# Kernel tuning notes

Hardware: AMD Instinct MI355X
Metric: run time of the kernel (lower is better)

The kernel has to match this reference:

```python
import jax, jax.numpy as jnp
import numpy as np

D_MODEL = 1024
NUM_HEADS = 16
SEQ_LEN = 2048
BATCH = 2
THETA = 10000.0


def apply_rope(x, positions, theta):
    # x: [..., seq, d_k]; positions: [seq]
    dk = x.shape[-1]
    half = dk // 2
    k = jnp.arange(half, dtype=jnp.float32)
    inv_freq = theta ** (-2.0 * k / dk)                 # [half]
    ang = positions.astype(jnp.float32)[:, None] * inv_freq  # [seq, half]
    cos, sin = jnp.cos(ang), jnp.sin(ang)
    xe = x[..., 0::2]   # even members of adjacent pairs
    xo = x[..., 1::2]
    out_e = cos * xe - sin * xo
    out_o = sin * xe + cos * xo
    # interleave pairs back: [..., seq, half, 2] -> [..., seq, dk]
    return jnp.stack([out_e, out_o], axis=-1).reshape(x.shape)


def setup_inputs() -> dict:
    key = jax.random.key(0)
    kx, kq, kk, kv, ko = jax.random.split(key, 5)
    sig = 1.0 / np.sqrt(D_MODEL)
    def tn(k):
        return jnp.clip(jax.random.normal(k, (D_MODEL, D_MODEL), jnp.float32), -3.0, 3.0) * sig
    return {
        "x": jax.random.normal(kx, (BATCH, SEQ_LEN, D_MODEL), jnp.float32),
        "q_proj_weight": tn(kq),
        "k_proj_weight": tn(kk),
        "v_proj_weight": tn(kv),
        "o_proj_weight": tn(ko),
        "token_positions": jnp.arange(SEQ_LEN, dtype=jnp.int32),
    }


def reference(x, q_proj_weight, k_proj_weight, v_proj_weight, o_proj_weight, token_positions):
    h = NUM_HEADS
    d = x.shape[-1]
    dh = d // h
    seq = x.shape[-2]
    Wq = q_proj_weight.reshape(h, dh, d)
    Wk = k_proj_weight.reshape(h, dh, d)
    Wv = v_proj_weight.reshape(h, dh, d)
    Q = jnp.einsum('bsd,hed->bhse', x, Wq)
    K = jnp.einsum('bsd,hed->bhse', x, Wk)
    V = jnp.einsum('bsd,hed->bhse', x, Wv)
    Q = apply_rope(Q, token_positions, THETA)
    K = apply_rope(K, token_positions, THETA)
    scores = jnp.einsum('bhqe,bhke->bhqk', Q, K) / jnp.sqrt(jnp.float32(dh))
    mask = jnp.tril(jnp.ones((seq, seq), dtype=bool))
    scores = jnp.where(mask, scores, -jnp.inf)
    probs = jax.nn.softmax(scores, axis=-1)
    att = jnp.einsum('bhqk,bhke->bhqe', probs, V)       # [b, h, s, dh]
    att = att.transpose(0, 2, 1, 3).reshape(x.shape[0], seq, d)  # concat heads
    return jnp.einsum('bsh,dh->bsd', att, o_proj_weight)
```

## Files before the change

### kernel.cpp

```cpp
#include <hip/hip_runtime.h>
#include <hip/hip_bf16.h>
#include <cstdint>
#include <cstddef>

#define DEV static __device__ __forceinline__

typedef __bf16 bf16x8 __attribute__((ext_vector_type(8)));
typedef float f32x4 __attribute__((ext_vector_type(4)));
typedef unsigned short u16;

static constexpr int BATCH = 2, SEQ = 2048, DM = 1024, NH = 16, DH = 64;
static constexpr int Kdim = 1024;
static constexpr int BS = BATCH * SEQ;

DEV u16 f2b(float f) {
  uint32_t u = __builtin_bit_cast(uint32_t, f);
  u += 0x7FFFu + ((u >> 16) & 1u);
  return (u16)(u >> 16);
}

DEV void gload_lds16(const void* g, void* l) {
  __builtin_amdgcn_global_load_lds((const __attribute__((address_space(1))) void*)g,
                                   (__attribute__((address_space(3))) void*)l, 16, 0, 0);
}

DEV void plswap32(uint32_t& a, uint32_t& b) {
  asm("v_permlane32_swap_b32 %0, %1" : "+v"(a), "+v"(b));
}
DEV void plswap16(uint32_t& a, uint32_t& b) {
  asm("v_permlane16_swap_b32 %0, %1" : "+v"(a), "+v"(b));
}

__global__ __launch_bounds__(256) void cast_all(const float* __restrict__ x,
    const float* __restrict__ wq, const float* __restrict__ wk,
    const float* __restrict__ wv, const float* __restrict__ wo,
    const int* __restrict__ pos,
    u16* __restrict__ xb, u16* __restrict__ wqb, u16* __restrict__ wkb,
    u16* __restrict__ wvb, u16* __restrict__ wob, float2* __restrict__ tab) {
  const int NX = (BATCH * SEQ * DM) / 4;
  const int NW = (DM * DM) / 4;
  const int NT = SEQ * 32;
  int i = blockIdx.x * blockDim.x + threadIdx.x;
  const int stride = gridDim.x * blockDim.x;
  for (; i < NX + 4 * NW + NT; i += stride) {
    if (i < NX + 4 * NW) {
      const float* src; u16* dst; int off;
      if (i < NX) { src = x; dst = xb; off = i; }
      else {
        const int j = i - NX, seg = j >> 18;
        off = j & (NW - 1);
        src = seg == 0 ? wq : seg == 1 ? wk : seg == 2 ? wv : wo;
        dst = seg == 0 ? wqb : seg == 1 ? wkb : seg == 2 ? wvb : wob;
      }
      float4 v = ((const float4*)src)[off];
      ushort4 o;
      o.x = f2b(v.x); o.y = f2b(v.y); o.z = f2b(v.z); o.w = f2b(v.w);
      ((ushort4*)dst)[off] = o;
    } else {
      const int t = i - NX - 4 * NW;
      const int s = t >> 5, j = t & 31;
      const float ang = (float)pos[s] * exp2f((float)j * -0.4152410118609203f);
      float sn, cs;
      sincosf(ang, &sn, &cs);
      tab[t] = make_float2(cs, sn);
    }
  }
}

template <bool OUTF32>
DEV void gemm_core64(const u16* __restrict__ A, const u16* __restrict__ Bm,
                     void* __restrict__ Cout, int ldC, int m0, int n0,
                     u16* __restrict__ As, u16* __restrict__ Bs) {
  const int tid = threadIdx.x;
  const int lane = tid & 63, wid = tid >> 6;
  const int wr = (wid >> 1) * 64, wc = (wid & 1) * 32;
  const int frow = lane & 15, fgrp = lane >> 4;
  constexpr int NK = Kdim / 32;
  f32x4 acc[4][2] = {};

  const int c0 = tid, c1 = tid + 256;
  const int ra0 = c0 >> 2, sa0 = (c0 & 3) ^ ((ra0 >> 1) & 3);
  const int ra1 = c1 >> 2, sa1 = (c1 & 3) ^ ((ra1 >> 1) & 3);
  const size_t gA0 = (size_t)(m0 + ra0) * Kdim + sa0 * 8;
  const size_t gA1 = (size_t)(m0 + ra1) * Kdim + sa1 * 8;
  const size_t gB0 = (size_t)(n0 + ra0) * Kdim + sa0 * 8;

#define GSTAGE(bufi, kofs)                                                      \
  do {                                                                          \
    gload_lds16(A + gA0 + (kofs), As + (bufi) * 4096 + wid * 512);              \
    gload_lds16(A + gA1 + (kofs), As + (bufi) * 4096 + wid * 512 + 2048);       \
    gload_lds16(Bm + gB0 + (kofs), Bs + (bufi) * 2048 + wid * 512);             \
  } while (0)

  GSTAGE(0, 0);
  for (int kt = 0; kt < NK; ++kt) {
    const int buf = kt & 1;
    if (kt + 1 < NK) {
      GSTAGE((kt + 1) & 1, (kt + 1) * 32);
      asm volatile("s_waitcnt vmcnt(3)" ::: "memory");
    } else {
      asm volatile("s_waitcnt vmcnt(0)" ::: "memory");
    }
    __builtin_amdgcn_s_barrier();

    bf16x8 af[4], bfr[2];
#pragma unroll
    for (int i = 0; i < 4; ++i) {
      const int ra = wr + i * 16 + frow;
      af[i] = *(const bf16x8*)((const char*)(As + buf * 4096) + ra * 64 +
                               ((fgrp ^ ((ra >> 1) & 3)) * 16));
    }
#pragma unroll
    for (int f = 0; f < 2; ++f) {
      const int rb = wc + f * 16 + frow;
      bfr[f] = *(const bf16x8*)((const char*)(Bs + buf * 2048) + rb * 64 +
                                ((fgrp ^ ((rb >> 1) & 3)) * 16));
    }
#pragma unroll
    for (int mi = 0; mi < 4; ++mi)
#pragma unroll
      for (int f = 0; f < 2; ++f)
        acc[mi][f] = __builtin_amdgcn_mfma_f32_16x16x32_bf16(af[mi], bfr[f], acc[mi][f], 0, 0, 0);

    __builtin_amdgcn_s_barrier();
  }
#undef GSTAGE

  const int colb = n0 + wc + frow;
  const int rowb = m0 + wr + fgrp * 4;
#pragma unroll
  for (int mi = 0; mi < 4; ++mi)
#pragma unroll
    for (int f = 0; f < 2; ++f)
#pragma unroll
      for (int r = 0; r < 4; ++r) {
        const int row = rowb + mi * 16 + r;
        const int col = colb + f * 16;
        const float v = acc[mi][f][r];
        if (OUTF32) ((float*)Cout)[(size_t)row * ldC + col] = v;
        else        ((u16*)Cout)[(size_t)row * ldC + col] = f2b(v);
      }
}

DEV void qk_core(const u16* __restrict__ xb, const u16* __restrict__ wq,
                 const u16* __restrict__ wk, u16* __restrict__ Qb, u16* __restrict__ Kb,
                 const float2* __restrict__ tab, int m0, int n0,
                 u16* __restrict__ As, u16* __restrict__ Bq, u16* __restrict__ Bk) {
  const int tid = threadIdx.x;
  const int lane = tid & 63, wid = tid >> 6;
  const int wr = (wid >> 1) * 64, wc = (wid & 1) * 32;
  const int frow = lane & 15, fgrp = lane >> 4;
  constexpr int NK = Kdim / 32;
  f32x4 accQ[4][2] = {}, accK[4][2] = {};

  const int c0 = tid, c1 = tid + 256;
  const int ra0 = c0 >> 2, sa0 = (c0 & 3) ^ ((ra0 >> 1) & 3);
  const int ra1 = c1 >> 2, sa1 = (c1 & 3) ^ ((ra1 >> 1) & 3);
  const size_t gA0 = (size_t)(m0 + ra0) * Kdim + sa0 * 8;
  const size_t gA1 = (size_t)(m0 + ra1) * Kdim + sa1 * 8;
  const size_t gB0 = (size_t)(n0 + ra0) * Kdim + sa0 * 8;

#define QKSTAGE(bufi, kofs)                                                     \
  do {                                                                          \
    gload_lds16(xb + gA0 + (kofs), As + (bufi) * 4096 + wid * 512);             \
    gload_lds16(xb + gA1 + (kofs), As + (bufi) * 4096 + wid * 512 + 2048);      \
    gload_lds16(wq + gB0 + (kofs), Bq + (bufi) * 2048 + wid * 512);             \
    gload_lds16(wk + gB0 + (kofs), Bk + (bufi) * 2048 + wid * 512);             \
  } while (0)

  QKSTAGE(0, 0);
  for (int kt = 0; kt < NK; ++kt) {
    const int buf = kt & 1;
    if (kt + 1 < NK) {
      QKSTAGE((kt + 1) & 1, (kt + 1) * 32);
      asm volatile("s_waitcnt vmcnt(4)" ::: "memory");
    } else {
      asm volatile("s_waitcnt vmcnt(0)" ::: "memory");
    }
    __builtin_amdgcn_s_barrier();

    bf16x8 af[4], bq[2], bk[2];
#pragma unroll
    for (int i = 0; i < 4; ++i) {
      const int ra = wr + i * 16 + frow;
      af[i] = *(const bf16x8*)((const char*)(As + buf * 4096) + ra * 64 +
                               ((fgrp ^ ((ra >> 1) & 3)) * 16));
    }
#pragma unroll
    for (int f2 = 0; f2 < 2; ++f2) {
      const int rb = wc + f2 * 16 + frow;
      const int off = rb * 64 + ((fgrp ^ ((rb >> 1) & 3)) * 16);
      bq[f2] = *(const bf16x8*)((const char*)(Bq + buf * 2048) + off);
      bk[f2] = *(const bf16x8*)((const char*)(Bk + buf * 2048) + off);
    }
#pragma unroll
    for (int mi = 0; mi < 4; ++mi)
#pragma unroll
      for (int f2 = 0; f2 < 2; ++f2) {
        accQ[mi][f2] = __builtin_amdgcn_mfma_f32_16x16x32_bf16(af[mi], bq[f2], accQ[mi][f2], 0, 0, 0);
        accK[mi][f2] = __builtin_amdgcn_mfma_f32_16x16x32_bf16(af[mi], bk[f2], accK[mi][f2], 0, 0, 0);
      }

    __builtin_amdgcn_s_barrier();
  }
#undef QKSTAGE

  const int colb = n0 + wc + frow;
  const int rowb = m0 + wr + fgrp * 4;
#pragma unroll
  for (int mi = 0; mi < 4; ++mi)
#pragma unroll
    for (int f2 = 0; f2 < 2; ++f2) {
      const int col = colb + f2 * 16;
      const int jj = (col & 63) >> 1;
      const int odd = col & 1;
#pragma unroll
      for (int r = 0; r < 4; ++r) {
        const int row = rowb + mi * 16 + r;
        const float2 cs_ = tab[(row & (SEQ - 1)) * 32 + jj];
        const float qv = accQ[mi][f2][r];
        const float qp = __shfl_xor(qv, 1);
        const float kv = accK[mi][f2][r];
        const float kp = __shfl_xor(kv, 1);
        float oq = odd ? fmaf(cs_.y, qp, cs_.x * qv) : fmaf(cs_.x, qv, -cs_.y * qp);
        float ok = odd ? fmaf(cs_.y, kp, cs_.x * kv) : fmaf(cs_.x, kv, -cs_.y * kp);
        oq *= 0.18033688011112043f;
        Qb[(size_t)row * DM + col] = f2b(oq);
        Kb[(size_t)row * DM + col] = f2b(ok);
      }
    }
}

__global__ __launch_bounds__(256) void gemm_proj(const u16* __restrict__ xb,
    const u16* __restrict__ wq, const u16* __restrict__ wk, const u16* __restrict__ wv,
    u16* __restrict__ Qb, u16* __restrict__ Kb, u16* __restrict__ Vtb,
    const float2* __restrict__ tab) {
  __shared__ u16 As[2][4096], B1[2][2048], B2[2][2048];
  const int g = blockIdx.x;
  if (g < 512) {
    const int xcd = g & 7, j = g >> 3;
    const int m0 = (xcd * 4 + (j >> 4)) * 128, n0 = (j & 15) * 64;
    qk_core(xb, wq, wk, Qb, Kb, tab, m0, n0, &As[0][0], &B1[0][0], &B2[0][0]);
  } else {
    const int f = g - 512;
    const int xcd = f & 7, j = f >> 3;
    const int m0 = xcd * 128, n0 = j * 64;
    gemm_core64<false>(wv, xb, Vtb, BS, m0, n0, &As[0][0], &B1[0][0]);
  }
}

__global__ __launch_bounds__(256) void gemm_o(const u16* __restrict__ attb,
                                              const u16* __restrict__ wob,
                                              float* __restrict__ out) {
  __shared__ u16 As[2][4096], Bs[2][2048];
  const int f = blockIdx.x;
  const int xcd = f & 7, k = f >> 3;
  const int grp = xcd * 8 + (k >> 3);
  const int m0 = (grp >> 1) * 128;
  const int n0 = ((grp & 1) * 8 + (k & 7)) * 64;
  gemm_core64<true>(attb, wob, out, DM, m0, n0, &As[0][0], &Bs[0][0]);
}

__global__ __launch_bounds__(256, 2) void attn_kernel(const u16* __restrict__ Qb,
                                                      const u16* __restrict__ Kb,
                                                      const u16* __restrict__ Vtb,
                                                      u16* __restrict__ attb) {
  __shared__ __align__(16) unsigned char SM[73728];
  u16* Qs = (u16*)(SM + 65536);
  float* Of = (float*)SM;
  float* Ld = (float*)(SM + 65536);

  const int tid = threadIdx.x, lane = tid & 63, wid = tid >> 6;
  const int flat = (int)blockIdx.x + 16 * (int)blockIdx.y;
  const int orig = (flat & 7) * 64 + (flat >> 3);
  const int xq = orig & 15;
  const int bh = orig >> 4;
  const int b = bh >> 4, h = bh & 15;
  const size_t base_bh = ((size_t)b * SEQ) * DM + h * DH;
  const int frow = lane & 15, fgrp = lane >> 4;
  const int w32 = wid * 32;
  const int swz = (frow & 7) << 4;

  const u16* Ksrcs[4];
  const u16* Vsrcs[4];
#pragma unroll
  for (int i = 0; i < 4; ++i) {
    const int c = tid + i * 256;
    const int rk = c >> 3, s8 = (c & 7) ^ (rk & 7);
    Ksrcs[i] = Kb + base_bh + (size_t)rk * DM + s8 * 8;
    const int rv = c >> 4, s16 = (c & 15) ^ (rv & 7);
    Vsrcs[i] = Vtb + (size_t)(h * DH + rv) * BS + (size_t)b * SEQ + s16 * 8;
  }
  const int cq0 = tid, cq1 = tid + 256;
  const int rq0 = cq0 >> 3, sq0 = (cq0 & 7) ^ (rq0 & 7);
  const int rq1 = cq1 >> 3, sq1 = (cq1 & 7) ^ (rq1 & 7);

#pragma unroll 1
  for (int phase = 0; phase < 2; ++phase) {
    const int qt = phase ? xq : 31 - xq;
    const int q0 = qt * 64;
    const int nkv = (qt >> 1) + 1;

    gload_lds16(Qb + base_bh + (size_t)(q0 + rq0) * DM + sq0 * 8, (char*)SM + 65536 + tid * 16);
    gload_lds16(Qb + base_bh + (size_t)(q0 + rq1) * DM + sq1 * 8, (char*)SM + 69632 + tid * 16);
#pragma unroll
    for (int i = 0; i < 4; ++i) {
      gload_lds16(Ksrcs[i], (char*)SM + wid * 1024 + i * 4096);
      gload_lds16(Vsrcs[i], (char*)SM + 32768 + wid * 1024 + i * 4096);
    }
    __syncthreads();

    bf16x8 qf[4][2];
#pragma unroll
    for (int qs = 0; qs < 4; ++qs)
#pragma unroll
      for (int ks = 0; ks < 2; ++ks) {
        const int byte = ((qs * 16 + frow) * 128 + ks * 64 + fgrp * 16) ^ swz;
        qf[qs][ks] = *(const bf16x8*)((const char*)Qs + byte);
      }

    f32x4 accO[4][4] = {};
    float l_lane[4] = {0.f, 0.f, 0.f, 0.f};

    const u16* Kp[4];
    const u16* Vp[4];
#pragma unroll
    for (int i = 0; i < 4; ++i) { Kp[i] = Ksrcs[i] + (size_t)128 * DM; Vp[i] = Vsrcs[i] + 128; }

    for (int kt = 0; kt < nkv; ++kt) {
      const char* Kc = (const char*)SM + (kt & 1) * 16384;
      const char* Vc = (const char*)SM + 32768 + (kt & 1) * 16384;
      if (kt + 1 < nkv) {
        const int nb = (kt + 1) & 1;
#pragma unroll
        for (int i = 0; i < 4; ++i) {
          gload_lds16(Kp[i], (char*)SM + nb * 16384 + wid * 1024 + i * 4096);
          gload_lds16(Vp[i], (char*)SM + 32768 + nb * 16384 + wid * 1024 + i * 4096);
          Kp[i] += (size_t)128 * DM;
          Vp[i] += 128;
        }
      }

      f32x4 sc[4][2] = {};
      __builtin_amdgcn_s_setprio(1);
#pragma unroll
      for (int tc = 0; tc < 2; ++tc)
#pragma unroll
        for (int ks = 0; ks < 2; ++ks) {
          const int byte = ((w32 + tc * 16 + frow) * 128 + ks * 64 + fgrp * 16) ^ swz;
          const bf16x8 kf = *(const bf16x8*)(Kc + byte);
#pragma unroll
          for (int qs = 0; qs < 4; ++qs)
            sc[qs][tc] = __builtin_amdgcn_mfma_f32_16x16x32_bf16(kf, qf[qs][ks], sc[qs][tc], 0, 0, 0);
        }
      __builtin_amdgcn_s_setprio(0);

      if (kt == nkv - 1) {
        const int kv0 = kt * 128;
#pragma unroll
        for (int qs = 0; qs < 4; ++qs)
#pragma unroll
          for (int tc = 0; tc < 2; ++tc)
#pragma unroll
            for (int r = 0; r < 4; ++r)
              if (kv0 + w32 + tc * 16 + fgrp * 4 + r > q0 + qs * 16 + frow)
                sc[qs][tc][r] = -1e30f;
      }

      bf16x8 pf[4];
#pragma unroll
      for (int qs = 0; qs < 4; ++qs) {
        const float p00 = exp2f(sc[qs][0][0]), p01 = exp2f(sc[qs][0][1]);
        const float p02 = exp2f(sc[qs][0][2]), p03 = exp2f(sc[qs][0][3]);
        const float p10 = exp2f(sc[qs][1][0]), p11 = exp2f(sc[qs][1][1]);
        const float p12 = exp2f(sc[qs][1][2]), p13 = exp2f(sc[qs][1][3]);
        l_lane[qs] += ((p00 + p01) + (p02 + p03)) + ((p10 + p11) + (p12 + p13));
        union { __bf16 bb[2]; uint32_t uu; } c00, c01, c10, c11;
        c00.bb[0] = (__bf16)p00; c00.bb[1] = (__bf16)p01;
        c01.bb[0] = (__bf16)p02; c01.bb[1] = (__bf16)p03;
        c10.bb[0] = (__bf16)p10; c10.bb[1] = (__bf16)p11;
        c11.bb[0] = (__bf16)p12; c11.bb[1] = (__bf16)p13;
        uint32_t a0 = c00.uu, a1 = c01.uu, b0 = c10.uu, b1 = c11.uu;
        plswap32(a0, b0); plswap16(a0, b0);
        plswap32(a1, b1); plswap16(a1, b1);
        union { uint32_t w[4]; bf16x8 v; } pk;
        pk.w[0] = a0; pk.w[1] = a1; pk.w[2] = b0; pk.w[3] = b1;
        pf[qs] = pk.v;
      }

      __builtin_amdgcn_s_setprio(1);
#pragma unroll
      for (int te = 0; te < 4; ++te) {
        const int byte = ((te * 16 + frow) * 256 + wid * 64 + fgrp * 16) ^ swz;
        const bf16x8 vf = *(const bf16x8*)(Vc + byte);
#pragma unroll
        for (int qs = 0; qs < 4; ++qs)
          accO[qs][te] = __builtin_amdgcn_mfma_f32_16x16x32_bf16(pf[qs], vf, accO[qs][te], 0, 0, 0);
      }
      __builtin_amdgcn_s_setprio(0);
      __syncthreads();
    }

    float* myOf = Of + wid * 4096;
#pragma unroll
    for (int qs = 0; qs < 4; ++qs)
#pragma unroll
      for (int te = 0; te < 4; ++te)
#pragma unroll
        for (int r = 0; r < 4; ++r)
          myOf[(qs * 16 + fgrp * 4 + r) * 64 + te * 16 + frow] = accO[qs][te][r];
#pragma unroll
    for (int qs = 0; qs < 4; ++qs) {
      l_lane[qs] += __shfl_xor(l_lane[qs], 16);
      l_lane[qs] += __shfl_xor(l_lane[qs], 32);
    }
    if (fgrp == 0) {
#pragma unroll
      for (int qs = 0; qs < 4; ++qs) Ld[wid * 64 + qs * 16 + frow] = l_lane[qs];
    }
    __syncthreads();

    {
      const int qlb = wid * 16 + fgrp * 4;
#pragma unroll
      for (int i = 0; i < 4; ++i) {
        const int ql = qlb + i;
        f32x4 s = {};
#pragma unroll
        for (int wv = 0; wv < 4; ++wv) {
          const f32x4 t = *(const f32x4*)(Of + wv * 4096 + ql * 64 + frow * 4);
          s += t;
        }
        const float lq = ((Ld[ql] + Ld[64 + ql]) + (Ld[128 + ql] + Ld[192 + ql]));
        const float inv = 1.0f / lq;
        ushort4 o;
        o.x = f2b(s[0] * inv); o.y = f2b(s[1] * inv);
        o.z = f2b(s[2] * inv); o.w = f2b(s[3] * inv);
        *(ushort4*)(attb + base_bh + (size_t)(q0 + ql) * DM + frow * 4) = o;
      }
    }
    __syncthreads();
  }
}

extern "C" void kernel_launch(void* const* d_in, const int* in_sizes, int n_in,
                              void* d_out, int out_size, void* d_ws, size_t ws_size,
                              hipStream_t stream) {
  const float* x  = (const float*)d_in[0];
  const float* wq = (const float*)d_in[1];
  const float* wk = (const float*)d_in[2];
  const float* wv = (const float*)d_in[3];
  const float* wo = (const float*)d_in[4];
  const int* pos  = (const int*)d_in[5];
  float* out = (float*)d_out;
  (void)in_sizes; (void)n_in; (void)out_size; (void)ws_size;

  char* ws = (char*)d_ws;
  const size_t MB = 1024 * 1024;
  u16* xb   = (u16*)(ws);
  u16* wqb  = (u16*)(ws + 8 * MB);
  u16* wkb  = (u16*)(ws + 10 * MB);
  u16* wvb  = (u16*)(ws + 12 * MB);
  u16* wob  = (u16*)(ws + 14 * MB);
  u16* Qb   = (u16*)(ws + 16 * MB);
  u16* Kb   = (u16*)(ws + 24 * MB);
  u16* Vtb  = (u16*)(ws + 32 * MB);
  u16* attb = (u16*)(ws + 40 * MB);
  float2* tab = (float2*)(ws + 40 * MB);

  cast_all<<<2048, 256, 0, stream>>>(x, wq, wk, wv, wo, pos, xb, wqb, wkb, wvb, wob, tab);
  gemm_proj<<<1024, 256, 0, stream>>>(xb, wqb, wkb, wvb, Qb, Kb, Vtb, tab);
  attn_kernel<<<dim3(16, 32), 256, 0, stream>>>(Qb, Kb, Vtb, attb);
  gemm_o<<<512, 256, 0, stream>>>(attb, wob, out);
}
```

Baseline: 112.4 us.

## Single-buffer K/V tiles and halve LDS to raise attention occupancy

Shrinks the attention kernel's shared memory from 72KB to 40KB by dropping K/V double buffering, aliasing Q into the reduction area, and splitting the cross-wave output reduction into two halves. Launch bounds go from 2 to 4 blocks per CU, so more waves are resident to hide latency. In exchange, the next K/V tile is loaded only after compute with an extra barrier, so global loads no longer overlap the MFMA work within a block. Register pressure also tightens under the higher launch bound.

```diff
diff --git a/kernel.cpp b/kernel.cpp
--- a/kernel.cpp
+++ b/kernel.cpp
@@ -261,14 +261,13 @@
   gemm_core64<true>(attb, wob, out, DM, m0, n0, &As[0][0], &Bs[0][0]);
 }
 
-__global__ __launch_bounds__(256, 2) void attn_kernel(const u16* __restrict__ Qb,
+__global__ __launch_bounds__(256, 4) void attn_kernel(const u16* __restrict__ Qb,
                                                       const u16* __restrict__ Kb,
                                                       const u16* __restrict__ Vtb,
                                                       u16* __restrict__ attb) {
-  __shared__ __align__(16) unsigned char SM[73728];
-  u16* Qs = (u16*)(SM + 65536);
+  __shared__ __align__(16) unsigned char SM[40960];
   float* Of = (float*)SM;
-  float* Ld = (float*)(SM + 65536);
+  float* Ld = (float*)(SM + 32768);
 
   const int tid = threadIdx.x, lane = tid & 63, wid = tid >> 6;
   const int flat = (int)blockIdx.x + 16 * (int)blockIdx.y;
@@ -301,12 +300,12 @@
     const int q0 = qt * 64;
     const int nkv = (qt >> 1) + 1;
 
-    gload_lds16(Qb + base_bh + (size_t)(q0 + rq0) * DM + sq0 * 8, (char*)SM + 65536 + tid * 16);
-    gload_lds16(Qb + base_bh + (size_t)(q0 + rq1) * DM + sq1 * 8, (char*)SM + 69632 + tid * 16);
+    gload_lds16(Qb + base_bh + (size_t)(q0 + rq0) * DM + sq0 * 8, (char*)SM + 32768 + wid * 1024);
+    gload_lds16(Qb + base_bh + (size_t)(q0 + rq1) * DM + sq1 * 8, (char*)SM + 32768 + wid * 1024 + 4096);
 #pragma unroll
     for (int i = 0; i < 4; ++i) {
       gload_lds16(Ksrcs[i], (char*)SM + wid * 1024 + i * 4096);
-      gload_lds16(Vsrcs[i], (char*)SM + 32768 + wid * 1024 + i * 4096);
+      gload_lds16(Vsrcs[i], (char*)SM + 16384 + wid * 1024 + i * 4096);
     }
     __syncthreads();
 
@@ -316,31 +315,16 @@
 #pragma unroll
       for (int ks = 0; ks < 2; ++ks) {
         const int byte = ((qs * 16 + frow) * 128 + ks * 64 + fgrp * 16) ^ swz;
-        qf[qs][ks] = *(const bf16x8*)((const char*)Qs + byte);
+        qf[qs][ks] = *(const bf16x8*)((const char*)SM + 32768 + byte);
       }
 
     f32x4 accO[4][4] = {};
     float l_lane[4] = {0.f, 0.f, 0.f, 0.f};
 
-    const u16* Kp[4];
-    const u16* Vp[4];
-#pragma unroll
-    for (int i = 0; i < 4; ++i) { Kp[i] = Ksrcs[i] + (size_t)128 * DM; Vp[i] = Vsrcs[i] + 128; }
+    const char* Kc = (const char*)SM;
+    const char* Vc = (const char*)SM + 16384;
 
     for (int kt = 0; kt < nkv; ++kt) {
-      const char* Kc = (const char*)SM + (kt & 1) * 16384;
-      const char* Vc = (const char*)SM + 32768 + (kt & 1) * 16384;
-      if (kt + 1 < nkv) {
-        const int nb = (kt + 1) & 1;
-#pragma unroll
-        for (int i = 0; i < 4; ++i) {
-          gload_lds16(Kp[i], (char*)SM + nb * 16384 + wid * 1024 + i * 4096);
-          gload_lds16(Vp[i], (char*)SM + 32768 + nb * 16384 + wid * 1024 + i * 4096);
-          Kp[i] += (size_t)128 * DM;
-          Vp[i] += 128;
-        }
-      }
-
       f32x4 sc[4][2] = {};
       __builtin_amdgcn_s_setprio(1);
 #pragma unroll
@@ -399,47 +383,60 @@
       }
       __builtin_amdgcn_s_setprio(0);
       __syncthreads();
-    }
-
-    float* myOf = Of + wid * 4096;
-#pragma unroll
-    for (int qs = 0; qs < 4; ++qs)
-#pragma unroll
-      for (int te = 0; te < 4; ++te)
-#pragma unroll
-        for (int r = 0; r < 4; ++r)
-          myOf[(qs * 16 + fgrp * 4 + r) * 64 + te * 16 + frow] = accO[qs][te][r];
+
+      if (kt + 1 < nkv) {
+        const size_t kvn = (size_t)(kt + 1) * 128;
+#pragma unroll
+        for (int i = 0; i < 4; ++i) {
+          gload_lds16(Ksrcs[i] + kvn * DM, (char*)SM + wid * 1024 + i * 4096);
+          gload_lds16(Vsrcs[i] + kvn, (char*)SM + 16384 + wid * 1024 + i * 4096);
+        }
+        __syncthreads();
+      }
+    }
+
 #pragma unroll
     for (int qs = 0; qs < 4; ++qs) {
       l_lane[qs] += __shfl_xor(l_lane[qs], 16);
       l_lane[qs] += __shfl_xor(l_lane[qs], 32);
     }
-    if (fgrp == 0) {
-#pragma unroll
-      for (int qs = 0; qs < 4; ++qs) Ld[wid * 64 + qs * 16 + frow] = l_lane[qs];
-    }
-    __syncthreads();
-
-    {
-      const int qlb = wid * 16 + fgrp * 4;
-#pragma unroll
-      for (int i = 0; i < 4; ++i) {
-        const int ql = qlb + i;
+#pragma unroll 1
+    for (int hh = 0; hh < 2; ++hh) {
+      float* myOf = Of + wid * 2048;
+#pragma unroll
+      for (int q2 = 0; q2 < 2; ++q2) {
+        const int qs = hh * 2 + q2;
+#pragma unroll
+        for (int te = 0; te < 4; ++te)
+#pragma unroll
+          for (int r = 0; r < 4; ++r)
+            myOf[(q2 * 16 + fgrp * 4 + r) * 64 + te * 16 + frow] = accO[qs][te][r];
+      }
+      if (fgrp == 0) {
+#pragma unroll
+        for (int q2 = 0; q2 < 2; ++q2)
+          Ld[wid * 32 + q2 * 16 + frow] = l_lane[hh * 2 + q2];
+      }
+      __syncthreads();
+
+#pragma unroll
+      for (int ii = 0; ii < 2; ++ii) {
+        const int qll = wid * 8 + fgrp * 2 + ii;
         f32x4 s = {};
+        float lq = 0.f;
 #pragma unroll
         for (int wv = 0; wv < 4; ++wv) {
-          const f32x4 t = *(const f32x4*)(Of + wv * 4096 + ql * 64 + frow * 4);
-          s += t;
+          s += *(const f32x4*)(Of + wv * 2048 + qll * 64 + frow * 4);
+          lq += Ld[wv * 32 + qll];
         }
-        const float lq = ((Ld[ql] + Ld[64 + ql]) + (Ld[128 + ql] + Ld[192 + ql]));
         const float inv = 1.0f / lq;
         ushort4 o;
         o.x = f2b(s[0] * inv); o.y = f2b(s[1] * inv);
         o.z = f2b(s[2] * inv); o.w = f2b(s[3] * inv);
-        *(ushort4*)(attb + base_bh + (size_t)(q0 + ql) * DM + frow * 4) = o;
-      }
-    }
-    __syncthreads();
+        *(ushort4*)(attb + base_bh + (size_t)(q0 + hh * 32 + qll) * DM + frow * 4) = o;
+      }
+      __syncthreads();
+    }
   }
 }
 
```

Result: slower. 250.4 us (+122.8%).
